# Optimization experiments

Hardware: AMD Instinct MI355X
Metric: run time of the kernel (lower is better)

The kernel has to match this reference:

```python
import jax, jax.numpy as jnp
import numpy as np

V, D, H, L, S = 50257, 1024, 16, 4, 4096
DH = D // H  # 64
DF = 4 * D   # 4096


def _layernorm(x, g, b, eps=1e-5):
    m = jnp.mean(x, axis=-1, keepdims=True)
    v = jnp.mean(jnp.square(x - m), axis=-1, keepdims=True)
    return (x - m) / jnp.sqrt(v + eps) * g + b


def _pos_encoding(s, d):
    # standard sinusoidal positional encoding [s, d]
    pos = jnp.arange(s, dtype=jnp.float32)[:, None]
    i = jnp.arange(d // 2, dtype=jnp.float32)[None, :]
    ang = pos * jnp.exp(-(2.0 * i / d) * jnp.log(10000.0))
    return jnp.concatenate([jnp.sin(ang), jnp.cos(ang)], axis=-1)


def setup_inputs() -> dict:
    key = jax.random.key(0)
    ks = jax.random.split(key, 8)
    s = 0.02
    return {
        "tokens": jax.random.randint(ks[0], (S,), 0, V),
        "emb": jax.random.normal(ks[1], (V, D), jnp.float32) * s,
        "Wq": jax.random.normal(ks[2], (L, H, D, DH), jnp.float32) * s,
        "bq": jnp.zeros((L, H, DH), jnp.float32),
        "Wk": jax.random.normal(ks[3], (L, H, D, DH), jnp.float32) * s,
        "bk": jnp.zeros((L, H, DH), jnp.float32),
        "Wv": jax.random.normal(ks[4], (L, H, D, DH), jnp.float32) * s,
        "bv": jnp.zeros((L, H, DH), jnp.float32),
        "ln1_g": jnp.ones((L, D), jnp.float32),
        "ln1_b": jnp.zeros((L, D), jnp.float32),
        "W1": jax.random.normal(ks[5], (L, D, DF), jnp.float32) * s,
        "b1": jnp.zeros((L, DF), jnp.float32),
        "W2": jax.random.normal(ks[6], (L, DF, D), jnp.float32) * s,
        "b2": jnp.zeros((L, D), jnp.float32),
        "ln2_g": jnp.ones((L, D), jnp.float32),
        "ln2_b": jnp.zeros((L, D), jnp.float32),
        "Wout": jax.random.normal(ks[7], (D, V), jnp.float32) * s,
        "bout": jnp.zeros((V,), jnp.float32),
    }


def reference(tokens, emb, Wq, bq, Wk, bk, Wv, bv, ln1_g, ln1_b,
              W1, b1, W2, b2, ln2_g, ln2_b, Wout, bout):
    x = emb[tokens] + _pos_encoding(S, D)          # [S, D]
    scale = 1.0 / jnp.sqrt(jnp.float32(DH))
    for l in range(L):
        # per-head projections: [H, S, DH]
        q = jnp.einsum("sd,hde->hse", x, Wq[l]) + bq[l][:, None, :]
        k = jnp.einsum("sd,hde->hse", x, Wk[l]) + bk[l][:, None, :]
        v = jnp.einsum("sd,hde->hse", x, Wv[l]) + bv[l][:, None, :]
        att = jax.nn.softmax(jnp.einsum("hse,hte->hst", q, k) * scale, axis=-1)
        y = jnp.einsum("hst,hte->hse", att, v)      # [H, S, DH]
        y = jnp.transpose(y, (1, 0, 2)).reshape(S, D)  # concat heads
        x = _layernorm(x + y, ln1_g[l], ln1_b[l])
        y = jnp.maximum(x @ W1[l] + b1[l], 0.0) @ W2[l] + b2[l]  # FFN
        x = _layernorm(x + y, ln2_g[l], ln2_b[l])
    logits = x @ Wout + bout                        # [S, V]
    return jax.nn.softmax(logits, axis=-1)
```

## Files before the change

kernel.cpp:

```cpp
#include <hip/hip_runtime.h>
#include <math.h>

#define S_LEN  4096
#define DMODEL 1024
#define NHEAD  16
#define DHEAD  64
#define DFF    4096
#define NLAYER 4
#define VOCAB  50257
#define NCBP   400

typedef unsigned short ushort_t;
typedef __attribute__((ext_vector_type(8))) __bf16 bf16x8;
typedef __attribute__((ext_vector_type(4))) float f32x4;

static __device__ __forceinline__ ushort_t f2bf(float f) {
  union { float f; unsigned u; } x; x.f = f;
  unsigned r = x.u + 0x7fffu + ((x.u >> 16) & 1u);
  return (ushort_t)(r >> 16);
}
static __device__ __forceinline__ float bf2f(ushort_t h) {
  union { unsigned u; float f; } x; x.u = ((unsigned)h) << 16;
  return x.f;
}
static __device__ __forceinline__ float exp2fast(float x) {
  return __builtin_amdgcn_exp2f(x);
}

#define GLOAD_LDS16(gp, lp) \
  __builtin_amdgcn_global_load_lds((const __attribute__((address_space(1))) void*)(gp), \
                                   (__attribute__((address_space(3))) void*)(lp), 16, 0, 0)

#define QSCALE 0.18033688011112042f

__global__ __launch_bounds__(256) void embed_kernel(
    const int* __restrict__ tokens, const float* __restrict__ emb,
    float* __restrict__ x, ushort_t* __restrict__ xh)
{
  int s = blockIdx.x;
  int tok = tokens[s];
  int d0 = threadIdx.x * 4;
  const double lf = 0.01798894603901598653;
  float4 ev = *(const float4*)(emb + (size_t)tok * DMODEL + d0);
  float o[4]; float evr[4] = {ev.x, ev.y, ev.z, ev.w};
  #pragma unroll
  for (int j = 0; j < 4; ++j) {
    int d = d0 + j;
    int i = (d < 512) ? d : d - 512;
    double ang = (double)s * exp(-lf * (double)i);
    float pe = (d < 512) ? (float)sin(ang) : (float)cos(ang);
    o[j] = evr[j] + pe;
  }
  *(float4*)(x + (size_t)s * DMODEL + d0) = make_float4(o[0], o[1], o[2], o[3]);
  ushort_t hv[4];
  #pragma unroll
  for (int j = 0; j < 4; ++j) hv[j] = f2bf(o[j]);
  *(ushort4*)(xh + (size_t)s * DMODEL + d0) = make_ushort4(hv[0], hv[1], hv[2], hv[3]);
}

__global__ __launch_bounds__(256)
void transpose_split(const float* __restrict__ in, ushort_t* __restrict__ oh,
                     ushort_t* __restrict__ ol,
                     long in_zstr, long out_zoff, long in_z2str, long out_z2off,
                     int zdiv, int in_rstride, int Kout, int Nvalid)
{
  __shared__ float tile[64][65];
  int z1 = blockIdx.z % zdiv, z2 = blockIdx.z / zdiv;
  long ioff = (long)z1 * in_zstr + (long)z2 * in_z2str;
  long ooff = (long)z1 * out_zoff + (long)z2 * out_z2off;
  const float* inz = in + ioff;
  ushort_t* ohz = oh + ooff;
  ushort_t* olz = ol + ooff;
  int k0 = blockIdx.x * 64, n0 = blockIdx.y * 64;
  int t = threadIdx.x;
  #pragma unroll
  for (int i = 0; i < 4; ++i) {
    int idx = t + i * 256;
    int kk = idx >> 4, c4 = idx & 15;
    #pragma unroll
    for (int j = 0; j < 4; ++j) {
      int n = n0 + c4 * 4 + j;
      float v = (n < Nvalid) ? inz[(long)(k0 + kk) * in_rstride + n] : 0.f;
      tile[c4 * 4 + j][kk] = v;
    }
  }
  __syncthreads();
  #pragma unroll
  for (int i = 0; i < 4; ++i) {
    int idx = t + i * 256;
    int nn = idx >> 4, k4 = idx & 15;
    ushort_t hv[4], lv[4];
    #pragma unroll
    for (int j = 0; j < 4; ++j) {
      float v = tile[nn][k4 * 4 + j];
      hv[j] = f2bf(v);
      lv[j] = f2bf(v - bf2f(hv[j]));
    }
    long ob = (long)(n0 + nn) * Kout + k0 + k4 * 4;
    *(ushort4*)(ohz + ob) = make_ushort4(hv[0], hv[1], hv[2], hv[3]);
    *(ushort4*)(olz + ob) = make_ushort4(lv[0], lv[1], lv[2], lv[3]);
  }
}

__global__ __launch_bounds__(256)
void transpose_h(const float* __restrict__ in, ushort_t* __restrict__ oh,
                 int in_rstride, int Kout, int Nvalid)
{
  __shared__ float tile[64][65];
  int k0 = blockIdx.x * 64, n0 = blockIdx.y * 64;
  int t = threadIdx.x;
  #pragma unroll
  for (int i = 0; i < 4; ++i) {
    int idx = t + i * 256;
    int kk = idx >> 4, c4 = idx & 15;
    #pragma unroll
    for (int j = 0; j < 4; ++j) {
      int n = n0 + c4 * 4 + j;
      float v = (n < Nvalid) ? in[(long)(k0 + kk) * in_rstride + n] : 0.f;
      tile[c4 * 4 + j][kk] = v;
    }
  }
  __syncthreads();
  #pragma unroll
  for (int i = 0; i < 4; ++i) {
    int idx = t + i * 256;
    int nn = idx >> 4, k4 = idx & 15;
    ushort_t hv[4];
    #pragma unroll
    for (int j = 0; j < 4; ++j) hv[j] = f2bf(tile[nn][k4 * 4 + j]);
    long ob = (long)(n0 + nn) * Kout + k0 + k4 * 4;
    *(ushort4*)(oh + ob) = make_ushort4(hv[0], hv[1], hv[2], hv[3]);
  }
}

__global__ __launch_bounds__(256)
void concat3_kernel(const float* __restrict__ a, const float* __restrict__ b,
                    const float* __restrict__ c, float* __restrict__ o,
                    int n, long lstrA, long lstrO)
{
  int i = blockIdx.x * 256 + threadIdx.x;
  long l = blockIdx.y;
  if (i < n) {
    o[l * lstrO + i]         = a[l * lstrA + i];
    o[l * lstrO + n + i]     = b[l * lstrA + i];
    o[l * lstrO + 2 * n + i] = c[l * lstrA + i];
  }
}

template<int EPI, bool RELU>
__global__ __launch_bounds__(512, 2)
void gemm8p(const ushort_t* __restrict__ Ah,
            const ushort_t* __restrict__ Bh, const ushort_t* __restrict__ Bl,
            const float* __restrict__ bias, float* __restrict__ C,
            ushort_t* __restrict__ O0, ushort_t* __restrict__ O1,
            ushort_t* __restrict__ O2, ushort_t* __restrict__ O4,
            int K, int ldk, long ldc, long czStride)
{
  constexpr int BUFSTR = 3 * 8192;
  constexpr int OBH = 8192, OBL = 16384;
  __shared__ ushort_t lds[2 * BUFSTR];

  const int t = threadIdx.x;
  const int l = t & 63;
  const int w = t >> 6;
  const int wr = w >> 2;
  const int wc = w & 3;
  const int lrow = l & 15;
  const int lk = (l >> 4) * 8;
  const int l8 = l * 8;
  const long m0 = (long)blockIdx.x * 256;
  const long n0 = (long)blockIdx.y * 256;
  const long kz = (long)blockIdx.z * K;

  const ushort_t *agp[2], *bgp[2], *blgp[2];
  int dst[2];
  #pragma unroll
  for (int i = 0; i < 2; ++i) {
    int s = i * 8 + w;
    dst[i] = s * 512 + l8;
    agp[i]  = Ah + (m0 + s * 16 + lrow) * (long)ldk + kz + lk;
    bgp[i]  = Bh + (n0 + s * 16 + lrow) * (long)ldk + kz + lk;
    blgp[i] = Bl + (n0 + s * 16 + lrow) * (long)ldk + kz + lk;
  }

  f32x4 acc[8][4];
  #pragma unroll
  for (int m = 0; m < 8; ++m)
    #pragma unroll
    for (int n = 0; n < 4; ++n) acc[m][n] = (f32x4)0.f;

  GLOAD_LDS16(agp[0],  &lds[dst[0]]);
  GLOAD_LDS16(agp[1],  &lds[dst[1]]);
  GLOAD_LDS16(bgp[0],  &lds[OBH + dst[0]]);
  GLOAD_LDS16(bgp[1],  &lds[OBH + dst[1]]);
  GLOAD_LDS16(blgp[0], &lds[OBL + dst[0]]);
  GLOAD_LDS16(blgp[1], &lds[OBL + dst[1]]);

  const int nk = K >> 5;
  int cur = 0;
  for (int kt = 0; kt < nk; ++kt) {
    const int knx = (kt + 1 < nk) ? (kt + 1) * 32 : 0;
    ushort_t* cb = &lds[cur * BUFSTR];
    ushort_t* nb = &lds[(cur ^ 1) * BUFSTR];
    bf16x8 af[8], bhf[4], blf[4];

    asm volatile("s_waitcnt vmcnt(2)" ::: "memory");
    __builtin_amdgcn_sched_barrier(0);
    __builtin_amdgcn_s_barrier();
    __builtin_amdgcn_sched_barrier(0);
    #pragma unroll
    for (int m = 0; m < 8; ++m)
      af[m] = *(const bf16x8*)&cb[(wr * 8 + m) * 512 + l8];
    #pragma unroll
    for (int n = 0; n < 4; ++n)
      bhf[n] = *(const bf16x8*)&cb[OBH + (wc * 4 + n) * 512 + l8];
    GLOAD_LDS16(agp[0] + knx, &nb[dst[0]]);
    GLOAD_LDS16(agp[1] + knx, &nb[dst[1]]);
    GLOAD_LDS16(bgp[0] + knx, &nb[OBH + dst[0]]);
    __builtin_amdgcn_s_setprio(1);
    #pragma unroll
    for (int m = 0; m < 8; ++m)
      #pragma unroll
      for (int n = 0; n < 4; ++n)
        acc[m][n] = __builtin_amdgcn_mfma_f32_16x16x32_bf16(af[m], bhf[n], acc[m][n], 0, 0, 0);
    __builtin_amdgcn_s_setprio(0);
    __builtin_amdgcn_sched_barrier(0);

    asm volatile("s_waitcnt vmcnt(3)" ::: "memory");
    __builtin_amdgcn_sched_barrier(0);
    __builtin_amdgcn_s_barrier();
    __builtin_amdgcn_sched_barrier(0);
    #pragma unroll
    for (int n = 0; n < 4; ++n)
      blf[n] = *(const bf16x8*)&cb[OBL + (wc * 4 + n) * 512 + l8];
    GLOAD_LDS16(bgp[1] + knx,  &nb[OBH + dst[1]]);
    GLOAD_LDS16(blgp[0] + knx, &nb[OBL + dst[0]]);
    GLOAD_LDS16(blgp[1] + knx, &nb[OBL + dst[1]]);
    __builtin_amdgcn_s_setprio(1);
    #pragma unroll
    for (int m = 0; m < 8; ++m)
      #pragma unroll
      for (int n = 0; n < 4; ++n)
        acc[m][n] = __builtin_amdgcn_mfma_f32_16x16x32_bf16(af[m], blf[n], acc[m][n], 0, 0, 0);
    __builtin_amdgcn_s_setprio(0);
    __builtin_amdgcn_sched_barrier(0);
    cur ^= 1;
  }
  asm volatile("s_waitcnt vmcnt(0)" ::: "memory");

  if constexpr (EPI == 2) {
    #pragma unroll
    for (int n = 0; n < 4; ++n) {
      long col = n0 + wc * 64 + n * 16 + lrow;
      float bv = bias[col];
      #pragma unroll
      for (int m = 0; m < 8; ++m) {
        #pragma unroll
        for (int r = 0; r < 4; ++r) {
          long row = m0 + wr * 128 + m * 16 + (l >> 4) * 4 + r;
          float v = acc[m][n][r] + bv;
          int c = (int)col;
          if (c < 1024) {
            int hh = c >> 6, e = c & 63;
            float qv = v * QSCALE;
            ushort_t hi = f2bf(qv);
            size_t a = ((size_t)hh * S_LEN + row) * 64 + e;
            O0[a] = hi; O1[a] = f2bf(qv - bf2f(hi));
          } else if (c < 2048) {
            int cc = c - 1024;
            int hh = cc >> 6, e = cc & 63;
            size_t a = ((size_t)hh * S_LEN + row) * 64 + e;
            O2[a] = f2bf(v);
          } else {
            int cc = c - 2048;
            int hh = cc >> 6, e = cc & 63;
            size_t a = ((size_t)hh * DHEAD + e) * S_LEN + row;
            O4[a] = f2bf(v);
          }
        }
      }
    }
  } else if constexpr (EPI == 1) {
    #pragma unroll
    for (int n = 0; n < 4; ++n) {
      long col = n0 + wc * 64 + n * 16 + lrow;
      float bv = bias[col];
      #pragma unroll
      for (int m = 0; m < 8; ++m) {
        #pragma unroll
        for (int r = 0; r < 4; ++r) {
          long row = m0 + wr * 128 + m * 16 + (l >> 4) * 4 + r;
          float v = acc[m][n][r] + bv;
          if (RELU) v = fmaxf(v, 0.f);
          O0[row * ldc + col] = f2bf(v);
        }
      }
    }
  } else {
    float* Cz = C + (long)blockIdx.z * czStride;
    #pragma unroll
    for (int n = 0; n < 4; ++n) {
      long col = n0 + wc * 64 + n * 16 + lrow;
      #pragma unroll
      for (int m = 0; m < 8; ++m) {
        #pragma unroll
        for (int r = 0; r < 4; ++r) {
          long row = m0 + wr * 128 + m * 16 + (l >> 4) * 4 + r;
          Cz[row * ldc + col] = acc[m][n][r];
        }
      }
    }
  }
}

template<bool BOUND>
__global__ __launch_bounds__(512, 2)
void gemm1p(const ushort_t* __restrict__ Ah, const ushort_t* __restrict__ Bh,
            const float* __restrict__ bias, float* __restrict__ C,
            int K, int ldk, long ldc, int Nlimit,
            float* __restrict__ Ppart, int cbbase)
{
  constexpr int OB = 8192;
  constexpr int BUFSTR = 16384;
  __shared__ ushort_t lds[2 * BUFSTR];
  __shared__ float psum[1024];

  const int t = threadIdx.x;
  const int l = t & 63;
  const int w = t >> 6;
  const int wr = w >> 2;
  const int wc = w & 3;
  const int lrow = l & 15;
  const int lk = (l >> 4) * 8;
  const int l8 = l * 8;
  const long m0 = (long)blockIdx.x * 256;
  const long n0 = (long)blockIdx.y * 256;

  const ushort_t *agp[2], *bgp[2];
  int dst[2];
  #pragma unroll
  for (int i = 0; i < 2; ++i) {
    int s = i * 8 + w;
    dst[i] = s * 512 + l8;
    agp[i] = Ah + (m0 + s * 16 + lrow) * (long)ldk + lk;
    bgp[i] = Bh + (n0 + s * 16 + lrow) * (long)ldk + lk;
  }

  f32x4 acc[8][4];
  #pragma unroll
  for (int m = 0; m < 8; ++m)
    #pragma unroll
    for (int n = 0; n < 4; ++n) acc[m][n] = (f32x4)0.f;

  GLOAD_LDS16(agp[0], &lds[dst[0]]);
  GLOAD_LDS16(agp[1], &lds[dst[1]]);
  GLOAD_LDS16(bgp[0], &lds[OB + dst[0]]);
  GLOAD_LDS16(bgp[1], &lds[OB + dst[1]]);
  GLOAD_LDS16(agp[0] + 32, &lds[BUFSTR + dst[0]]);
  GLOAD_LDS16(agp[1] + 32, &lds[BUFSTR + dst[1]]);
  GLOAD_LDS16(bgp[0] + 32, &lds[BUFSTR + OB + dst[0]]);
  GLOAD_LDS16(bgp[1] + 32, &lds[BUFSTR + OB + dst[1]]);

  const int nk = K >> 5;
  int cur = 0;
  for (int kt = 0; kt < nk; ++kt) {
    ushort_t* cb = &lds[cur * BUFSTR];
    bf16x8 af[8], bhf[4];

    asm volatile("s_waitcnt vmcnt(4)" ::: "memory");
    __builtin_amdgcn_sched_barrier(0);
    __builtin_amdgcn_s_barrier();
    __builtin_amdgcn_sched_barrier(0);
    #pragma unroll
    for (int m = 0; m < 8; ++m)
      af[m] = *(const bf16x8*)&cb[(wr * 8 + m) * 512 + l8];
    #pragma unroll
    for (int n = 0; n < 4; ++n)
      bhf[n] = *(const bf16x8*)&cb[OB + (wc * 4 + n) * 512 + l8];
    __builtin_amdgcn_sched_barrier(0);
    asm volatile("s_waitcnt lgkmcnt(0)" ::: "memory");
    __builtin_amdgcn_sched_barrier(0);
    __builtin_amdgcn_s_barrier();
    __builtin_amdgcn_sched_barrier(0);
    const int knx2 = (kt + 2 < nk) ? (kt + 2) * 32 : 0;
    GLOAD_LDS16(agp[0] + knx2, &cb[dst[0]]);
    GLOAD_LDS16(agp[1] + knx2, &cb[dst[1]]);
    GLOAD_LDS16(bgp[0] + knx2, &cb[OB + dst[0]]);
    GLOAD_LDS16(bgp[1] + knx2, &cb[OB + dst[1]]);
    __builtin_amdgcn_s_setprio(1);
    #pragma unroll
    for (int m = 0; m < 8; ++m)
      #pragma unroll
      for (int n = 0; n < 4; ++n)
        acc[m][n] = __builtin_amdgcn_mfma_f32_16x16x32_bf16(af[m], bhf[n], acc[m][n], 0, 0, 0);
    __builtin_amdgcn_s_setprio(0);
    __builtin_amdgcn_sched_barrier(0);
    cur ^= 1;
  }
  asm volatile("s_waitcnt vmcnt(0)" ::: "memory");

  float smr[8][4];
  #pragma unroll
  for (int m = 0; m < 8; ++m)
    #pragma unroll
    for (int r = 0; r < 4; ++r) smr[m][r] = 0.f;
  #pragma unroll
  for (int n = 0; n < 4; ++n) {
    long col = n0 + wc * 64 + n * 16 + lrow;
    bool cok = (!BOUND) || (col < (long)Nlimit);
    float bv = cok ? bias[col] : 0.f;
    #pragma unroll
    for (int m = 0; m < 8; ++m) {
      #pragma unroll
      for (int r = 0; r < 4; ++r) {
        long row = m0 + wr * 128 + m * 16 + (l >> 4) * 4 + r;
        float e = cok ? __expf(acc[m][n][r] + bv) : 0.f;
        if (cok) C[row * ldc + col] = e;
        smr[m][r] += e;
      }
    }
  }
  #pragma unroll
  for (int m = 0; m < 8; ++m) {
    #pragma unroll
    for (int r = 0; r < 4; ++r) {
      float s = smr[m][r];
      s += __shfl_xor(s, 1);
      s += __shfl_xor(s, 2);
      s += __shfl_xor(s, 4);
      s += __shfl_xor(s, 8);
      if (lrow == 0)
        psum[wc * 256 + wr * 128 + m * 16 + (l >> 4) * 4 + r] = s;
    }
  }
  __syncthreads();
  if (t < 256) {
    float s = psum[t] + psum[256 + t] + psum[512 + t] + psum[768 + t];
    Ppart[(m0 + t) * NCBP + cbbase + blockIdx.y] = s;
  }
}

__global__ __launch_bounds__(256)
void attn_mfma(const ushort_t* __restrict__ qh, const ushort_t* __restrict__ ql,
               const ushort_t* __restrict__ kh, const ushort_t* __restrict__ vt,
               float* __restrict__ y)
{
  __shared__ ushort_t lds[24576];

  const int t = threadIdx.x, l = t & 63, w = t >> 6;
  const int lrow = l & 15, lhi = l >> 4;
  const int h = blockIdx.y;
  const int bw = blockIdx.x * 128 + w * 32;
  const size_t hS = (size_t)h * S_LEN * DHEAD;
  const size_t hV = (size_t)h * DHEAD * S_LEN;
  const int pb = 16384 + w * 2048;

  bf16x8 qhf[2][2], qlf[2][2];
  #pragma unroll
  for (int m = 0; m < 2; ++m)
    #pragma unroll
    for (int ks = 0; ks < 2; ++ks) {
      size_t a = hS + (size_t)(bw + m * 16 + lrow) * 64 + ks * 32 + lhi * 8;
      qhf[m][ks] = *(const bf16x8*)(qh + a);
      qlf[m][ks] = *(const bf16x8*)(ql + a);
    }

  f32x4 acc[2][4];
  #pragma unroll
  for (int m = 0; m < 2; ++m)
    #pragma unroll
    for (int n = 0; n < 4; ++n) acc[m][n] = (f32x4)0.f;
  float mrow[8], lsum[8];
  #pragma unroll
  for (int i = 0; i < 8; ++i) { mrow[i] = -1e30f; lsum[i] = 0.f; }

  #pragma unroll
  for (int i = 0; i < 2; ++i) {
    int s = i * 4 + w;
    size_t krow = (size_t)((s >> 1) * 16 + lrow);
    int koff = (s & 1) * 32 + lhi * 8;
    GLOAD_LDS16(kh + hS + krow * 64 + koff, &lds[s * 512 + l * 8]);
    int toff = (s & 1) * 32 + lhi * 8;
    GLOAD_LDS16(vt + hV + krow * S_LEN + toff, &lds[4096 + s * 512 + l * 8]);
  }

  int cur = 0;
  for (int kt = 0; kt < S_LEN; kt += 64) {
    asm volatile("s_waitcnt vmcnt(0)" ::: "memory");
    __builtin_amdgcn_sched_barrier(0);
    __builtin_amdgcn_s_barrier();
    __builtin_amdgcn_sched_barrier(0);
    ushort_t* cb = &lds[cur * 8192];
    if (kt + 64 < S_LEN) {
      ushort_t* nb = &lds[(cur ^ 1) * 8192];
      int kn = kt + 64;
      #pragma unroll
      for (int i = 0; i < 2; ++i) {
        int s = i * 4 + w;
        size_t krow = (size_t)(kn + (s >> 1) * 16 + lrow);
        int koff = (s & 1) * 32 + lhi * 8;
        GLOAD_LDS16(kh + hS + krow * 64 + koff, &nb[s * 512 + l * 8]);
        size_t erow = (size_t)((s >> 1) * 16 + lrow);
        int toff = kn + (s & 1) * 32 + lhi * 8;
        GLOAD_LDS16(vt + hV + erow * S_LEN + toff, &nb[4096 + s * 512 + l * 8]);
      }
    }

    f32x4 sacc[2][4];
    #pragma unroll
    for (int m = 0; m < 2; ++m)
      #pragma unroll
      for (int n = 0; n < 4; ++n) sacc[m][n] = (f32x4)0.f;
    #pragma unroll
    for (int ks = 0; ks < 2; ++ks) {
      bf16x8 bh_[4];
      #pragma unroll
      for (int n = 0; n < 4; ++n)
        bh_[n] = *(const bf16x8*)&cb[(n * 2 + ks) * 512 + l * 8];
      #pragma unroll
      for (int m = 0; m < 2; ++m)
        #pragma unroll
        for (int n = 0; n < 4; ++n) {
          sacc[m][n] = __builtin_amdgcn_mfma_f32_16x16x32_bf16(qhf[m][ks], bh_[n], sacc[m][n], 0, 0, 0);
          sacc[m][n] = __builtin_amdgcn_mfma_f32_16x16x32_bf16(qlf[m][ks], bh_[n], sacc[m][n], 0, 0, 0);
        }
    }

    float tmv[2][4];
    bool up = false;
    #pragma unroll
    for (int m = 0; m < 2; ++m) {
      #pragma unroll
      for (int r = 0; r < 4; ++r) {
        float tm = fmaxf(fmaxf(sacc[m][0][r], sacc[m][1][r]),
                         fmaxf(sacc[m][2][r], sacc[m][3][r]));
        tm = fmaxf(tm, __shfl_xor(tm, 1));
        tm = fmaxf(tm, __shfl_xor(tm, 2));
        tm = fmaxf(tm, __shfl_xor(tm, 4));
        tm = fmaxf(tm, __shfl_xor(tm, 8));
        tmv[m][r] = tm;
        up = up || (tm > mrow[m * 4 + r]);
      }
    }
    if (__ballot(up) != 0ULL) {
      #pragma unroll
      for (int m = 0; m < 2; ++m) {
        #pragma unroll
        for (int r = 0; r < 4; ++r) {
          const int idx = m * 4 + r;
          float mn = fmaxf(mrow[idx], tmv[m][r]);
          float al = exp2fast(mrow[idx] - mn);
          mrow[idx] = mn;
          lsum[idx] *= al;
          #pragma unroll
          for (int n = 0; n < 4; ++n) acc[m][n][r] *= al;
        }
      }
    }
    #pragma unroll
    for (int m = 0; m < 2; ++m) {
      #pragma unroll
      for (int r = 0; r < 4; ++r) {
        const int idx = m * 4 + r;
        float rs = 0.f;
        #pragma unroll
        for (int n = 0; n < 4; ++n) {
          float p = exp2fast(sacc[m][n][r] - mrow[idx]);
          rs += p;
          int pa = pb + ((m * 2 + (n >> 1)) << 9) + (((n & 1) * 2 + (lrow >> 3)) << 7)
                   + ((lhi * 4 + r) << 3) + (l & 7);
          pa ^= (lrow >> 3) << 3;
          lds[pa] = f2bf(p);
        }
        rs += __shfl_xor(rs, 1);
        rs += __shfl_xor(rs, 2);
        rs += __shfl_xor(rs, 4);
        rs += __shfl_xor(rs, 8);
        lsum[idx] += rs;
      }
    }

    #pragma unroll
    for (int ks = 0; ks < 2; ++ks) {
      bf16x8 pa_[2];
      #pragma unroll
      for (int m = 0; m < 2; ++m) {
        int ra = pb + ((m * 2 + ks) << 9) + (l << 3);
        ra ^= ((l >> 4) & 1) << 3;
        pa_[m] = *(const bf16x8*)&lds[ra];
      }
      #pragma unroll
      for (int n = 0; n < 4; ++n) {
        bf16x8 vf = *(const bf16x8*)&cb[4096 + (n * 2 + ks) * 512 + l * 8];
        #pragma unroll
        for (int m = 0; m < 2; ++m)
          acc[m][n] = __builtin_amdgcn_mfma_f32_16x16x32_bf16(pa_[m], vf, acc[m][n], 0, 0, 0);
      }
    }
    cur ^= 1;
  }

  #pragma unroll
  for (int m = 0; m < 2; ++m) {
    #pragma unroll
    for (int r = 0; r < 4; ++r) {
      float inv = 1.0f / lsum[m * 4 + r];
      int row = bw + m * 16 + lhi * 4 + r;
      #pragma unroll
      for (int n = 0; n < 4; ++n)
        y[(size_t)row * DMODEL + h * 64 + n * 16 + lrow] = acc[m][n][r] * inv;
    }
  }
}

__device__ __forceinline__ float block_sum256(float v, float* sm)
{
  #pragma unroll
  for (int off = 32; off >= 1; off >>= 1) v += __shfl_xor(v, off);
  int w = threadIdx.x >> 6;
  if ((threadIdx.x & 63) == 0) sm[w] = v;
  __syncthreads();
  v = sm[0] + sm[1] + sm[2] + sm[3];
  __syncthreads();
  return v;
}

__global__ __launch_bounds__(256)
void resid_ln_kernel(float* __restrict__ x, const float* __restrict__ y,
                     const float* __restrict__ g, const float* __restrict__ b,
                     ushort_t* __restrict__ xh)
{
  __shared__ float sm[4];
  int row = blockIdx.x, t = threadIdx.x;
  float4 xv = *(const float4*)(x + (size_t)row * DMODEL + t * 4);
  float4 yv = *(const float4*)(y + (size_t)row * DMODEL + t * 4);
  float a0 = xv.x + yv.x, a1 = xv.y + yv.y, a2 = xv.z + yv.z, a3 = xv.w + yv.w;
  float s = block_sum256(a0 + a1 + a2 + a3, sm);
  float mean = s * (1.0f / DMODEL);
  float d0 = a0 - mean, d1 = a1 - mean, d2 = a2 - mean, d3 = a3 - mean;
  float vs = block_sum256(d0*d0 + d1*d1 + d2*d2 + d3*d3, sm);
  float inv = rsqrtf(vs * (1.0f / DMODEL) + 1e-5f);
  float4 gv = *(const float4*)(g + t * 4);
  float4 bv = *(const float4*)(b + t * 4);
  float o[4];
  o[0] = d0 * inv * gv.x + bv.x;
  o[1] = d1 * inv * gv.y + bv.y;
  o[2] = d2 * inv * gv.z + bv.z;
  o[3] = d3 * inv * gv.w + bv.w;
  *(float4*)(x + (size_t)row * DMODEL + t * 4) = make_float4(o[0], o[1], o[2], o[3]);
  ushort_t hv[4];
  #pragma unroll
  for (int j = 0; j < 4; ++j) hv[j] = f2bf(o[j]);
  *(ushort4*)(xh + (size_t)row * DMODEL + t * 4) = make_ushort4(hv[0], hv[1], hv[2], hv[3]);
}

__global__ __launch_bounds__(256)
void resid_ln_red(float* __restrict__ x, const float* __restrict__ parts,
                  long pstride, const float* __restrict__ bias,
                  const float* __restrict__ g, const float* __restrict__ b,
                  ushort_t* __restrict__ xh)
{
  __shared__ float sm[4];
  int row = blockIdx.x, t = threadIdx.x;
  size_t base = (size_t)row * DMODEL + t * 4;
  float4 xv = *(const float4*)(x + base);
  float4 bb = *(const float4*)(bias + t * 4);
  float a0 = xv.x + bb.x, a1 = xv.y + bb.y, a2 = xv.z + bb.z, a3 = xv.w + bb.w;
  #pragma unroll
  for (int z = 0; z < 4; ++z) {
    float4 pv = *(const float4*)(parts + (size_t)z * pstride + base);
    a0 += pv.x; a1 += pv.y; a2 += pv.z; a3 += pv.w;
  }
  float s = block_sum256(a0 + a1 + a2 + a3, sm);
  float mean = s * (1.0f / DMODEL);
  float d0 = a0 - mean, d1 = a1 - mean, d2 = a2 - mean, d3 = a3 - mean;
  float vs = block_sum256(d0*d0 + d1*d1 + d2*d2 + d3*d3, sm);
  float inv = rsqrtf(vs * (1.0f / DMODEL) + 1e-5f);
  float4 gv = *(const float4*)(g + t * 4);
  float4 bv = *(const float4*)(b + t * 4);
  float o[4];
  o[0] = d0 * inv * gv.x + bv.x;
  o[1] = d1 * inv * gv.y + bv.y;
  o[2] = d2 * inv * gv.z + bv.z;
  o[3] = d3 * inv * gv.w + bv.w;
  *(float4*)(x + base) = make_float4(o[0], o[1], o[2], o[3]);
  ushort_t hv[4];
  #pragma unroll
  for (int j = 0; j < 4; ++j) hv[j] = f2bf(o[j]);
  *(ushort4*)(xh + base) = make_ushort4(hv[0], hv[1], hv[2], hv[3]);
}

__global__ __launch_bounds__(256)
void scale_softmax(float* __restrict__ out, const float* __restrict__ partials,
                   int ncb)
{
  __shared__ float sm[4];
  int row = blockIdx.x, t = threadIdx.x;
  float s = 0.f;
  for (int cb = t; cb < ncb; cb += 256) s += partials[(size_t)row * NCBP + cb];
  s = block_sum256(s, sm);
  float inv = 1.0f / s;
  float* p = out + (size_t)row * VOCAB;
  int head = (int)((((uintptr_t)16 - ((uintptr_t)p & 15)) & 15) >> 2);
  if (t < head) p[t] *= inv;
  int nvec = (VOCAB - head) >> 2;
  float4* pv = (float4*)(p + head);
  for (int i = t; i < nvec; i += 256) {
    float4 v = pv[i];
    v.x *= inv; v.y *= inv; v.z *= inv; v.w *= inv;
    pv[i] = v;
  }
  int done = head + nvec * 4;
  if (t < VOCAB - done) p[done + t] *= inv;
}

extern "C" void kernel_launch(void* const* d_in, const int* in_sizes, int n_in,
                              void* d_out, int out_size, void* d_ws, size_t ws_size,
                              hipStream_t stream)
{
  const int*   tokens = (const int*)  d_in[0];
  const float* emb    = (const float*)d_in[1];
  const float* Wq     = (const float*)d_in[2];
  const float* bq     = (const float*)d_in[3];
  const float* Wk     = (const float*)d_in[4];
  const float* bk     = (const float*)d_in[5];
  const float* Wv     = (const float*)d_in[6];
  const float* bv     = (const float*)d_in[7];
  const float* ln1g   = (const float*)d_in[8];
  const float* ln1b   = (const float*)d_in[9];
  const float* W1     = (const float*)d_in[10];
  const float* b1     = (const float*)d_in[11];
  const float* W2     = (const float*)d_in[12];
  const float* b2     = (const float*)d_in[13];
  const float* ln2g   = (const float*)d_in[14];
  const float* ln2b   = (const float*)d_in[15];
  const float* Wout   = (const float*)d_in[16];
  const float* bout   = (const float*)d_in[17];

  char* wsb = (char*)d_ws;
  ushort_t* xh     = (ushort_t*)(wsb);
  ushort_t* stripH = (ushort_t*)(wsb + ((size_t)8  << 20));
  float*    partials = (float*)(wsb + ((size_t)24 << 20));
  ushort_t* woutT  = (ushort_t*)(wsb + ((size_t)32 << 20));
  const bool bigws = ws_size >= ((size_t)137 << 20);

  char* ob = (char*)d_out;
  float*    x     = (float*)(ob);
  float*    yb    = (float*)(ob + ((size_t)16  << 20));
  ushort_t* qh    = (ushort_t*)(ob + ((size_t)32  << 20));
  ushort_t* ql    = (ushort_t*)(ob + ((size_t)40  << 20));
  ushort_t* kh    = (ushort_t*)(ob + ((size_t)48  << 20));
  ushort_t* vt    = (ushort_t*)(ob + ((size_t)56  << 20));
  ushort_t* h1h   = (ushort_t*)(ob + ((size_t)64  << 20));
  float*    fparts= (float*)(ob + ((size_t)96  << 20));
  ushort_t* wqkvhA= (ushort_t*)(ob + ((size_t)160 << 20));
  ushort_t* wqkvlA= (ushort_t*)(ob + ((size_t)184 << 20));
  ushort_t* w1hA  = (ushort_t*)(ob + ((size_t)208 << 20));
  ushort_t* w1lA  = (ushort_t*)(ob + ((size_t)240 << 20));
  ushort_t* w2hA  = (ushort_t*)(ob + ((size_t)272 << 20));
  ushort_t* w2lA  = (ushort_t*)(ob + ((size_t)304 << 20));
  float*    bqkvA = (float*)(ob + ((size_t)336 << 20));
  float*    outf  = (float*)d_out;

  const long WQKV_L = 3072L * 1024;
  const long WFF_L  = 4096L * 1024;

  embed_kernel<<<S_LEN, 256, 0, stream>>>(tokens, emb, x, xh);

  transpose_split<<<dim3(16, 1, 64), 256, 0, stream>>>(
      Wq, wqkvhA, wqkvlA,
      (long)DMODEL * DHEAD, (long)DHEAD * DMODEL,
      (long)NHEAD * DMODEL * DHEAD, WQKV_L,
      16, DHEAD, DMODEL, DHEAD);
  transpose_split<<<dim3(16, 1, 64), 256, 0, stream>>>(
      Wk, wqkvhA + 1024 * 1024, wqkvlA + 1024 * 1024,
      (long)DMODEL * DHEAD, (long)DHEAD * DMODEL,
      (long)NHEAD * DMODEL * DHEAD, WQKV_L,
      16, DHEAD, DMODEL, DHEAD);
  transpose_split<<<dim3(16, 1, 64), 256, 0, stream>>>(
      Wv, wqkvhA + 2048 * 1024, wqkvlA + 2048 * 1024,
      (long)DMODEL * DHEAD, (long)DHEAD * DMODEL,
      (long)NHEAD * DMODEL * DHEAD, WQKV_L,
      16, DHEAD, DMODEL, DHEAD);
  transpose_split<<<dim3(16, 64, 4), 256, 0, stream>>>(
      W1, w1hA, w1lA, 0, 0,
      (long)DMODEL * DFF, WFF_L, 1, DFF, DMODEL, DFF);
  transpose_split<<<dim3(64, 16, 4), 256, 0, stream>>>(
      W2, w2hA, w2lA, 0, 0,
      (long)DFF * DMODEL, WFF_L, 1, DMODEL, DFF, DMODEL);
  concat3_kernel<<<dim3(4, NLAYER), 256, 0, stream>>>(
      bq, bk, bv, bqkvA, 1024, 1024, 3072);

  for (int l = 0; l < NLAYER; ++l) {
    const ushort_t* wqh = wqkvhA + (long)l * WQKV_L;
    const ushort_t* wql = wqkvlA + (long)l * WQKV_L;
    const ushort_t* w1h = w1hA + (long)l * WFF_L;
    const ushort_t* w1l = w1lA + (long)l * WFF_L;
    const ushort_t* w2h = w2hA + (long)l * WFF_L;
    const ushort_t* w2l = w2lA + (long)l * WFF_L;

    gemm8p<2, false><<<dim3(16, 12), 512, 0, stream>>>(
        xh, wqh, wql, bqkvA + (long)l * 3072, nullptr,
        qh, ql, kh, vt, 1024, 1024, 0, 0);

    attn_mfma<<<dim3(32, 16), 256, 0, stream>>>(qh, ql, kh, vt, yb);

    resid_ln_kernel<<<S_LEN, 256, 0, stream>>>(x, yb,
        ln1g + (size_t)l * DMODEL, ln1b + (size_t)l * DMODEL, xh);

    gemm8p<1, true><<<dim3(16, 16), 512, 0, stream>>>(
        xh, w1h, w1l, b1 + (long)l * DFF, nullptr,
        h1h, nullptr, nullptr, nullptr, 1024, 1024, 4096, 0);
    gemm8p<0, false><<<dim3(16, 4, 4), 512, 0, stream>>>(
        h1h, w2h, w2l, nullptr, fparts,
        nullptr, nullptr, nullptr, nullptr,
        1024, 4096, 1024, (long)S_LEN * DMODEL);
    resid_ln_red<<<S_LEN, 256, 0, stream>>>(x, fparts, (long)S_LEN * DMODEL,
        b2 + (long)l * DMODEL,
        ln2g + (size_t)l * DMODEL, ln2b + (size_t)l * DMODEL, xh);
  }

  if (bigws) {
    transpose_h<<<dim3(16, 786, 1), 256, 0, stream>>>(
        Wout, woutT, VOCAB, DMODEL, VOCAB);
    gemm1p<true><<<dim3(16, 197), 512, 0, stream>>>(
        xh, woutT, bout, outf, 1024, 1024, VOCAB, VOCAB, partials, 0);
  } else {
    const int SW = 4096;
    for (int is = 0; is < 12; ++is) {
      int n0 = is * SW;
      transpose_h<<<dim3(16, 64, 1), 256, 0, stream>>>(
          Wout + n0, stripH, VOCAB, DMODEL, SW);
      gemm1p<false><<<dim3(16, 16), 512, 0, stream>>>(
          xh, stripH, bout + n0, outf + n0,
          1024, 1024, VOCAB, SW, partials, is * 16);
    }
    int n0 = 12 * SW;
    int ncols = VOCAB - n0;
    int nt64 = (ncols + 63) / 64;
    int nb256 = (ncols + 255) / 256;
    transpose_h<<<dim3(16, nt64, 1), 256, 0, stream>>>(
        Wout + n0, stripH, VOCAB, DMODEL, ncols);
    gemm1p<true><<<dim3(16, nb256), 512, 0, stream>>>(
        xh, stripH, bout + n0, outf + n0,
        1024, 1024, VOCAB, ncols, partials, 12 * 16);
  }
  const int ncb = (VOCAB + 255) / 256;
  scale_softmax<<<S_LEN, 256, 0, stream>>>(outf, partials, ncb);
}
```

Before: 3.704 ms.

## Triple-buffer LDS in logits GEMM and reorder epilogue stores row-wise

The vocab-projection GEMM moves from double to triple LDS buffering. Each iteration's prefetch now targets the buffer read two steps earlier, so the second workgroup barrier and the LDS-drain wait before issuing global loads are removed. The GEMM epilogues are also restructured to hoist column indices and biases and loop over rows outermost, so the stores for a row are issued together. The change raises static LDS to roughly 100KB per block, which may stop two 512-thread blocks from sharing a CU and lower occupancy.

```diff
diff --git a/kernel.cpp b/kernel.cpp
--- a/kernel.cpp
+++ b/kernel.cpp
@@ -281,33 +281,39 @@
       }
     }
   } else if constexpr (EPI == 1) {
+    long col4[4]; float bv4[4];
     #pragma unroll
     for (int n = 0; n < 4; ++n) {
-      long col = n0 + wc * 64 + n * 16 + lrow;
-      float bv = bias[col];
-      #pragma unroll
-      for (int m = 0; m < 8; ++m) {
+      col4[n] = n0 + wc * 64 + n * 16 + lrow;
+      bv4[n] = bias[col4[n]];
+    }
+    #pragma unroll
+    for (int m = 0; m < 8; ++m) {
+      #pragma unroll
+      for (int r = 0; r < 4; ++r) {
+        long row = m0 + wr * 128 + m * 16 + (l >> 4) * 4 + r;
+        ushort_t* crow = O0 + row * ldc;
         #pragma unroll
-        for (int r = 0; r < 4; ++r) {
-          long row = m0 + wr * 128 + m * 16 + (l >> 4) * 4 + r;
-          float v = acc[m][n][r] + bv;
+        for (int n = 0; n < 4; ++n) {
+          float v = acc[m][n][r] + bv4[n];
           if (RELU) v = fmaxf(v, 0.f);
-          O0[row * ldc + col] = f2bf(v);
+          crow[col4[n]] = f2bf(v);
         }
       }
     }
   } else {
     float* Cz = C + (long)blockIdx.z * czStride;
-    #pragma unroll
-    for (int n = 0; n < 4; ++n) {
-      long col = n0 + wc * 64 + n * 16 + lrow;
-      #pragma unroll
-      for (int m = 0; m < 8; ++m) {
+    long col4[4];
+    #pragma unroll
+    for (int n = 0; n < 4; ++n) col4[n] = n0 + wc * 64 + n * 16 + lrow;
+    #pragma unroll
+    for (int m = 0; m < 8; ++m) {
+      #pragma unroll
+      for (int r = 0; r < 4; ++r) {
+        long row = m0 + wr * 128 + m * 16 + (l >> 4) * 4 + r;
+        float* crow = Cz + row * ldc;
         #pragma unroll
-        for (int r = 0; r < 4; ++r) {
-          long row = m0 + wr * 128 + m * 16 + (l >> 4) * 4 + r;
-          Cz[row * ldc + col] = acc[m][n][r];
-        }
+        for (int n = 0; n < 4; ++n) crow[col4[n]] = acc[m][n][r];
       }
     }
   }
@@ -322,7 +328,7 @@
 {
   constexpr int OB = 8192;
   constexpr int BUFSTR = 16384;
-  __shared__ ushort_t lds[2 * BUFSTR];
+  __shared__ ushort_t lds[3 * BUFSTR];
   __shared__ float psum[1024];
 
   const int t = threadIdx.x;
@@ -365,6 +371,8 @@
   int cur = 0;
   for (int kt = 0; kt < nk; ++kt) {
     ushort_t* cb = &lds[cur * BUFSTR];
+    int nxt = cur + 2; if (nxt >= 3) nxt -= 3;
+    ushort_t* nb = &lds[nxt * BUFSTR];
     bf16x8 af[8], bhf[4];
 
     asm volatile("s_waitcnt vmcnt(4)" ::: "memory");
@@ -377,16 +385,11 @@
     #pragma unroll
     for (int n = 0; n < 4; ++n)
       bhf[n] = *(const bf16x8*)&cb[OB + (wc * 4 + n) * 512 + l8];
-    __builtin_amdgcn_sched_barrier(0);
-    asm volatile("s_waitcnt lgkmcnt(0)" ::: "memory");
-    __builtin_amdgcn_sched_barrier(0);
-    __builtin_amdgcn_s_barrier();
-    __builtin_amdgcn_sched_barrier(0);
     const int knx2 = (kt + 2 < nk) ? (kt + 2) * 32 : 0;
-    GLOAD_LDS16(agp[0] + knx2, &cb[dst[0]]);
-    GLOAD_LDS16(agp[1] + knx2, &cb[dst[1]]);
-    GLOAD_LDS16(bgp[0] + knx2, &cb[OB + dst[0]]);
-    GLOAD_LDS16(bgp[1] + knx2, &cb[OB + dst[1]]);
+    GLOAD_LDS16(agp[0] + knx2, &nb[dst[0]]);
+    GLOAD_LDS16(agp[1] + knx2, &nb[dst[1]]);
+    GLOAD_LDS16(bgp[0] + knx2, &nb[OB + dst[0]]);
+    GLOAD_LDS16(bgp[1] + knx2, &nb[OB + dst[1]]);
     __builtin_amdgcn_s_setprio(1);
     #pragma unroll
     for (int m = 0; m < 8; ++m)
@@ -395,7 +398,7 @@
         acc[m][n] = __builtin_amdgcn_mfma_f32_16x16x32_bf16(af[m], bhf[n], acc[m][n], 0, 0, 0);
     __builtin_amdgcn_s_setprio(0);
     __builtin_amdgcn_sched_barrier(0);
-    cur ^= 1;
+    cur = (cur == 2) ? 0 : cur + 1;
   }
   asm volatile("s_waitcnt vmcnt(0)" ::: "memory");
 
@@ -404,18 +407,23 @@
   for (int m = 0; m < 8; ++m)
     #pragma unroll
     for (int r = 0; r < 4; ++r) smr[m][r] = 0.f;
+  long col4[4]; float bv4[4]; bool cok4[4];
   #pragma unroll
   for (int n = 0; n < 4; ++n) {
-    long col = n0 + wc * 64 + n * 16 + lrow;
-    bool cok = (!BOUND) || (col < (long)Nlimit);
-    float bv = cok ? bias[col] : 0.f;
-    #pragma unroll
-    for (int m = 0; m < 8; ++m) {
-      #pragma unroll
-      for (int r = 0; r < 4; ++r) {
-        long row = m0 + wr * 128 + m * 16 + (l >> 4) * 4 + r;
-        float e = cok ? __expf(acc[m][n][r] + bv) : 0.f;
-        if (cok) C[row * ldc + col] = e;
+    col4[n] = n0 + wc * 64 + n * 16 + lrow;
+    cok4[n] = (!BOUND) || (col4[n] < (long)Nlimit);
+    bv4[n] = cok4[n] ? bias[col4[n]] : 0.f;
+  }
+  #pragma unroll
+  for (int m = 0; m < 8; ++m) {
+    #pragma unroll
+    for (int r = 0; r < 4; ++r) {
+      long row = m0 + wr * 128 + m * 16 + (l >> 4) * 4 + r;
+      float* crow = C + row * ldc;
+      #pragma unroll
+      for (int n = 0; n < 4; ++n) {
+        float e = cok4[n] ? __expf(acc[m][n][r] + bv4[n]) : 0.f;
+        if (cok4[n]) crow[col4[n]] = e;
         smr[m][r] += e;
       }
     }
```

New measurement: 3.214 ms, median of 3. 1.15x faster.
